# Kernel optimization log

Hardware: AMD Instinct MI355X
Metric: run time of the kernel (lower is better)

Reference implementation:

```python
import jax, jax.numpy as jnp
import numpy as np

L = 5          # num_layer
EMB = 128      # emb_dim
IN_DIM = 9     # input_dim
EDGE_DIM = 10
N_NODES = 50000
N_EDGES = 600000
N_GRAPHS = 512
BN_EPS = 1e-5


def _bn(x, g, b):
    # training-mode batch norm over axis 0 (biased variance, as torch)
    m = x.mean(axis=0)
    v = x.var(axis=0)
    return (x - m) * jax.lax.rsqrt(v + BN_EPS) * g + b


def setup_inputs() -> dict:
    key = jax.random.key(0)
    ks = jax.random.split(key, 20)
    s = 0.05
    d = {
        'x': jax.random.normal(ks[0], (N_NODES, IN_DIM), jnp.float32),
        'edge_index': jax.random.randint(ks[1], (2, N_EDGES), 0, N_NODES, jnp.int32),
        'edge_attr': jax.random.normal(ks[2], (N_EDGES, EDGE_DIM), jnp.float32),
        'batch': jnp.sort(jax.random.randint(ks[3], (N_NODES,), 0, N_GRAPHS, jnp.int32)),
        'node_W': jax.random.normal(ks[4], (IN_DIM, EMB)) * s,
        'node_b': jnp.zeros((EMB,)),
        'vn_emb': jnp.zeros((1, EMB)),                 # torch init: constant 0
        'eps': jnp.zeros((L,)),                        # GIN eps init 0
        'edge_W': jax.random.normal(ks[5], (L, EDGE_DIM, EMB)) * s,
        'edge_b': jnp.zeros((L, EMB)),
        'conv_W1': jax.random.normal(ks[6], (L, EMB, 2 * EMB)) * s,
        'conv_b1': jnp.zeros((L, 2 * EMB)),
        'conv_bn_g': jnp.ones((L, 2 * EMB)),
        'conv_bn_b': jnp.zeros((L, 2 * EMB)),
        'conv_W2': jax.random.normal(ks[7], (L, 2 * EMB, EMB)) * s,
        'conv_b2': jnp.zeros((L, EMB)),
        'bn_g': jnp.ones((L, EMB)),
        'bn_b': jnp.zeros((L, EMB)),
        'vmlp_W1': jax.random.normal(ks[8], (L - 1, EMB, 2 * EMB)) * s,
        'vmlp_b1': jnp.zeros((L - 1, 2 * EMB)),
        'vmlp_bn1_g': jnp.ones((L - 1, 2 * EMB)),
        'vmlp_bn1_b': jnp.zeros((L - 1, 2 * EMB)),
        'vmlp_W2': jax.random.normal(ks[9], (L - 1, 2 * EMB, EMB)) * s,
        'vmlp_b2': jnp.zeros((L - 1, EMB)),
        'vmlp_bn2_g': jnp.ones((L - 1, EMB)),
        'vmlp_bn2_b': jnp.zeros((L - 1, EMB)),
    }
    return d


def reference(x, edge_index, edge_attr, batch,
              node_W, node_b, vn_emb, eps, edge_W, edge_b,
              conv_W1, conv_b1, conv_bn_g, conv_bn_b, conv_W2, conv_b2,
              bn_g, bn_b,
              vmlp_W1, vmlp_b1, vmlp_bn1_g, vmlp_bn1_b,
              vmlp_W2, vmlp_b2, vmlp_bn2_g, vmlp_bn2_b):
    n = x.shape[0]
    src, dst = edge_index[0], edge_index[1]
    vn = jnp.broadcast_to(vn_emb[0], (N_GRAPHS, EMB))  # virtual node per graph
    h = x @ node_W + node_b                            # node encoder
    for l in range(L):
        h_in = h + vn[batch]                           # broadcast virtual node
        # DrugGINConv
        e = edge_attr @ edge_W[l] + edge_b[l]          # edge encoder [E,EMB]
        msg = jax.nn.relu(h_in[src] + e)               # gather + message
        agg = jax.ops.segment_sum(msg, dst, num_segments=n)  # scatter-add
        t = (1.0 + eps[l]) * h_in + agg
        t = _bn(t @ conv_W1[l] + conv_b1[l], conv_bn_g[l], conv_bn_b[l])
        t = jax.nn.relu(t) @ conv_W2[l] + conv_b2[l]
        t = _bn(t, bn_g[l], bn_b[l])                   # outer batch norm
        h = t if l == L - 1 else jax.nn.relu(t)        # dropout identity (p=0)
        if l < L - 1:
            vtmp = jax.ops.segment_sum(h_in, batch, num_segments=N_GRAPHS) + vn
            u = _bn(vtmp @ vmlp_W1[l] + vmlp_b1[l], vmlp_bn1_g[l], vmlp_bn1_b[l])
            u = jax.nn.relu(u) @ vmlp_W2[l] + vmlp_b2[l]
            vn = jax.nn.relu(_bn(u, vmlp_bn2_g[l], vmlp_bn2_b[l]))
    return h
```

## Files before the change

kernel.cpp:

```cpp
#include <hip/hip_runtime.h>


#define EMB 128
#define NGR 512
#define NLAYER 5
static constexpr float BN_EPS = 1e-5f;

typedef __attribute__((ext_vector_type(8))) short short8v;
typedef __attribute__((ext_vector_type(4))) float f32x4;

__device__ __forceinline__ ushort f2bf(float f) {
  union { float f; unsigned u; } c; c.f = f;
  return (ushort)((c.u + 0x7FFFu + ((c.u >> 16) & 1u)) >> 16);
}
__device__ __forceinline__ float bf2f(ushort h) {
  union { unsigned u; float f; } c; c.u = ((unsigned)h) << 16;
  return c.f;
}


__global__ void init_kernel(int* __restrict__ deg, int ndeg,
                            float* __restrict__ stats, int nstats,
                            float* __restrict__ vn, const float* __restrict__ vn_emb) {
  int idx = blockIdx.x * blockDim.x + threadIdx.x;
  if (idx < ndeg) deg[idx] = 0;
  if (idx < nstats) stats[idx] = 0.f;
  if (idx < NGR * EMB) vn[idx] = vn_emb[idx & (EMB - 1)];
}

__global__ void deg_kernel(const int* __restrict__ ei, int* __restrict__ deg, int E) {
  int e = blockIdx.x * blockDim.x + threadIdx.x;
  if (e < E) atomicAdd(&deg[ei[E + e]], 1);
}


__global__ void scan1_kernel(const int* __restrict__ deg, int* __restrict__ bsum, int n) {
  __shared__ int ws[4];
  int t = threadIdx.x;
  int base = blockIdx.x * 2048 + t * 8;
  int s = 0;
  #pragma unroll
  for (int i = 0; i < 8; ++i) {
    int idx = base + i;
    if (idx < n) s += deg[idx];
  }
  #pragma unroll
  for (int off = 32; off; off >>= 1) s += __shfl_down(s, off);
  if ((t & 63) == 0) ws[t >> 6] = s;
  __syncthreads();
  if (t == 0) bsum[blockIdx.x] = ws[0] + ws[1] + ws[2] + ws[3];
}

__global__ void scan2_kernel(const int* __restrict__ bsum, int* __restrict__ boff,
                             int* __restrict__ row_n, int nb) {
  int t = threadIdx.x;
  int mine = (t < nb) ? bsum[t] : 0;
  int v = mine;
  #pragma unroll
  for (int off = 1; off < 64; off <<= 1) {
    int u = __shfl_up(v, off);
    if (t >= off) v += u;
  }
  if (t < nb) boff[t] = v - mine;
  if (t == nb - 1) *row_n = v;
}

__global__ __launch_bounds__(256) void scan3_kernel(const int* __restrict__ deg,
                                                    const int* __restrict__ boff,
                                                    int* __restrict__ row_start,
                                                    int* __restrict__ cursor, int n) {
  __shared__ int lsum[256];
  int t = threadIdx.x;
  int base = blockIdx.x * 2048 + t * 8;
  int loc[8];
  int s = 0;
  #pragma unroll
  for (int i = 0; i < 8; ++i) {
    int idx = base + i;
    int d = (idx < n) ? deg[idx] : 0;
    loc[i] = s;
    s += d;
  }
  lsum[t] = s;
  __syncthreads();
  #pragma unroll
  for (int off = 1; off < 256; off <<= 1) {
    int v2 = (t >= off) ? lsum[t - off] : 0;
    __syncthreads();
    lsum[t] += v2;
    __syncthreads();
  }
  int toff = boff[blockIdx.x] + lsum[t] - s;
  #pragma unroll
  for (int i = 0; i < 8; ++i) {
    int idx = base + i;
    if (idx < n) {
      int rs = toff + loc[i];
      row_start[idx] = rs;
      cursor[idx] = rs;
    }
  }
}

__global__ void fill_kernel(const int* __restrict__ ei, int* __restrict__ cursor,
                            int2* __restrict__ el, int E) {
  int e = blockIdx.x * blockDim.x + threadIdx.x;
  if (e < E) {
    int d = ei[E + e];
    int pos = atomicAdd(&cursor[d], 1);
    el[pos] = make_int2(e, ei[e]);
  }
}

__global__ void bounds_kernel(const int* __restrict__ batch, int* __restrict__ gstart,
                              int n, int ng) {
  int g = blockIdx.x * blockDim.x + threadIdx.x;
  if (g > ng) return;
  int lo = 0, hi = n;
  while (lo < hi) {
    int mid = (lo + hi) >> 1;
    if (batch[mid] < g) lo = mid + 1; else hi = mid;
  }
  gstart[g] = lo;
}

__global__ void wtrans_kernel(const float* __restrict__ W, ushort* __restrict__ Wth,
                              ushort* __restrict__ Wtl, int K, int N, int total) {
  int idx = blockIdx.x * blockDim.x + threadIdx.x;
  if (idx >= total) return;
  int kk = idx % K;
  int t = idx / K;
  int nn = t % N;
  int l = t / N;
  float v = W[((size_t)l * K + kk) * N + nn];
  ushort h = f2bf(v);
  Wth[idx] = h;
  Wtl[idx] = f2bf(v - bf2f(h));
}

__global__ void encoder_kernel(const float* __restrict__ x, const float* __restrict__ W,
                               const float* __restrict__ b, float* __restrict__ h0, int n) {
  __shared__ float Ws[9][EMB];
  __shared__ float bs[EMB];
  int t = threadIdx.x;
  if (t < EMB) {
    #pragma unroll
    for (int k = 0; k < 9; ++k) Ws[k][t] = W[k * EMB + t];
    bs[t] = b[t];
  }
  __syncthreads();
  int total = n * EMB;
  for (int idx = blockIdx.x * blockDim.x + t; idx < total; idx += gridDim.x * blockDim.x) {
    int i = idx >> 7, j = idx & 127;
    const float* xr = x + i * 9;
    float acc = bs[j];
    #pragma unroll
    for (int k = 0; k < 9; ++k) acc = fmaf(xr[k], Ws[k][j], acc);
    h0[idx] = acc;
  }
}


template <bool RAW>
__global__ void hin_kernel(const float* __restrict__ src, const float* __restrict__ vn,
                           const int* __restrict__ batch, const float* __restrict__ s2raw,
                           const float* __restrict__ g2, const float* __restrict__ b2,
                           float* __restrict__ h_in, ushort* __restrict__ h16, int n) {
  __shared__ float sc[EMB], sh[EMB];
  if (!RAW) {
    int j = threadIdx.x;
    if (j < EMB) {
      float s = s2raw[j], q = s2raw[EMB + j];
      float mean = s / (float)n;
      float var = q / (float)n - mean * mean;
      float scl = g2[j] * rsqrtf(var + BN_EPS);
      sc[j] = scl;
      sh[j] = b2[j] - mean * scl;
    }
    __syncthreads();
  }
  int total = n * EMB;
  for (int idx = blockIdx.x * blockDim.x + threadIdx.x; idx < total; idx += gridDim.x * blockDim.x) {
    int i = idx >> 7, j = idx & 127;
    float v = src[idx];
    if (!RAW) v = fmaxf(fmaf(v, sc[j], sh[j]), 0.f);
    float hv = v + vn[batch[i] * EMB + j];
    h_in[idx] = hv;
    h16[idx] = f2bf(hv);
  }
}

__global__ void out_kernel(const float* __restrict__ t2, const float* __restrict__ s2raw,
                           const float* __restrict__ g2, const float* __restrict__ b2,
                           float* __restrict__ out, int n) {
  __shared__ float sc[EMB], sh[EMB];
  int j0 = threadIdx.x;
  if (j0 < EMB) {
    float s = s2raw[j0], q = s2raw[EMB + j0];
    float mean = s / (float)n;
    float var = q / (float)n - mean * mean;
    float scl = g2[j0] * rsqrtf(var + BN_EPS);
    sc[j0] = scl;
    sh[j0] = b2[j0] - mean * scl;
  }
  __syncthreads();
  int total = n * EMB;
  for (int idx = blockIdx.x * blockDim.x + threadIdx.x; idx < total; idx += gridDim.x * blockDim.x) {
    int j = idx & 127;
    out[idx] = fmaf(t2[idx], sc[j], sh[j]);
  }
}

__global__ void vnsum_kernel(const float* __restrict__ h_in, const int* __restrict__ gstart,
                             const float* __restrict__ vn, float* __restrict__ vnsum) {
  int g = blockIdx.x;
  int j = threadIdx.x;
  int s0 = gstart[g], s1 = gstart[g + 1];
  float acc = vn[g * EMB + j];
  for (int i = s0; i < s1; ++i) acc += h_in[i * EMB + j];
  vnsum[g * EMB + j] = acc;
}

__global__ __launch_bounds__(128) void agg_kernel(
    const float* __restrict__ h_in, const ushort* __restrict__ h16,
    const int* __restrict__ row_start, const int2* __restrict__ el,
    const float* __restrict__ edge_attr, const float* __restrict__ eW,
    const float* __restrict__ eb, const float* __restrict__ eps_p, int l,
    ushort* __restrict__ tpre_h, ushort* __restrict__ tpre_l, int n) {
  __shared__ float W[10][EMB];
  __shared__ float bia[EMB];
  int j = threadIdx.x;
  #pragma unroll
  for (int k = 0; k < 10; ++k) W[k][j] = eW[k * EMB + j];
  bia[j] = eb[j];
  float epsv = 1.f + eps_p[l];
  __syncthreads();

  int i = blockIdx.x;
  int s0 = row_start[i], s1 = row_start[i + 1];
  float acc = epsv * h_in[(size_t)i * EMB + j];
  int p = s0;
  for (; p + 4 <= s1; p += 4) {
    int2 e0 = el[p], e1 = el[p + 1], e2 = el[p + 2], e3 = el[p + 3];
    float hv0 = bf2f(h16[(size_t)e0.y * EMB + j]);
    float hv1 = bf2f(h16[(size_t)e1.y * EMB + j]);
    float hv2 = bf2f(h16[(size_t)e2.y * EMB + j]);
    float hv3 = bf2f(h16[(size_t)e3.y * EMB + j]);
    const float* ea0 = edge_attr + (size_t)e0.x * 10;
    const float* ea1 = edge_attr + (size_t)e1.x * 10;
    const float* ea2 = edge_attr + (size_t)e2.x * 10;
    const float* ea3 = edge_attr + (size_t)e3.x * 10;
    float v0 = bia[j], v1 = bia[j], v2 = bia[j], v3 = bia[j];
    #pragma unroll
    for (int k = 0; k < 10; ++k) {
      float w = W[k][j];
      v0 = fmaf(ea0[k], w, v0);
      v1 = fmaf(ea1[k], w, v1);
      v2 = fmaf(ea2[k], w, v2);
      v3 = fmaf(ea3[k], w, v3);
    }
    acc += fmaxf(v0 + hv0, 0.f) + fmaxf(v1 + hv1, 0.f) +
           fmaxf(v2 + hv2, 0.f) + fmaxf(v3 + hv3, 0.f);
  }
  for (; p < s1; ++p) {
    int2 e0 = el[p];
    float hv0 = bf2f(h16[(size_t)e0.y * EMB + j]);
    const float* ea0 = edge_attr + (size_t)e0.x * 10;
    float v0 = bia[j];
    #pragma unroll
    for (int k = 0; k < 10; ++k) v0 = fmaf(ea0[k], W[k][j], v0);
    acc += fmaxf(v0 + hv0, 0.f);
  }
  ushort hh = f2bf(acc);
  tpre_h[(size_t)i * EMB + j] = hh;
  tpre_l[(size_t)i * EMB + j] = f2bf(acc - bf2f(hh));
}

template <int KT, int NT, bool BN_A, bool STATS, bool APRE>
__global__ __launch_bounds__(256) void gemm_mfma(
    const float* __restrict__ A, const ushort* __restrict__ Ath,
    const ushort* __restrict__ Atl,
    const ushort* __restrict__ Bth, const ushort* __restrict__ Btl,
    const float* __restrict__ bias,
    float* __restrict__ C, int M,
    const float* __restrict__ bnraw, const float* __restrict__ bng,
    const float* __restrict__ bnb, float* __restrict__ statraw) {
  constexpr int BM = 128, BN = 128, BK = 32;
  constexpr int LDK = BK + 8;
  constexpr int KSTEPS = KT / BK;
  __shared__ ushort Ah[BM][LDK], Al[BM][LDK];
  __shared__ ushort Bh[BN][LDK], Bl[BN][LDK];
  __shared__ float red[8][BN], redq[8][BN];
  constexpr int SCN = BN_A ? KT : 1;
  __shared__ float scS[SCN], shS[SCN];

  int tid = threadIdx.x;
  if (BN_A) {
    for (int k = tid; k < KT; k += 256) {
      float s = bnraw[k], q = bnraw[KT + k];
      float mean = s / (float)M;
      float var = q / (float)M - mean * mean;
      float scl = bng[k] * rsqrtf(var + BN_EPS);
      scS[k] = scl;
      shS[k] = bnb[k] - mean * scl;
    }
  }

  int wv = tid >> 6, lane = tid & 63;
  int wr = wv >> 1, wc = wv & 1;
  int lr = lane & 15, kg = lane >> 4;
  int bm0 = blockIdx.x * BM;
  int gc0 = blockIdx.y * BN;

  int sr = tid >> 1;
  int skq = (tid & 1) * 16;

  f32x4 acc[4][4];
  #pragma unroll
  for (int fm = 0; fm < 4; ++fm)
    #pragma unroll
    for (int fn = 0; fn < 4; ++fn) {
      float b = bias[gc0 + wc * 64 + fn * 16 + lr];
      acc[fm][fn][0] = b; acc[fm][fn][1] = b; acc[fm][fn][2] = b; acc[fm][fn][3] = b;
    }

  for (int kt = 0; kt < KSTEPS; ++kt) {
    __syncthreads();
    {
      int grow = bm0 + sr;
      if (APRE) {
        short8v z;
        #pragma unroll
        for (int q2 = 0; q2 < 8; ++q2) z[q2] = 0;
        if (grow < M) {
          const ushort* aph = Ath + (size_t)grow * KT + kt * BK + skq;
          const ushort* apl = Atl + (size_t)grow * KT + kt * BK + skq;
          *(short8v*)&Ah[sr][skq] = *(const short8v*)aph;
          *(short8v*)&Ah[sr][skq + 8] = *(const short8v*)(aph + 8);
          *(short8v*)&Al[sr][skq] = *(const short8v*)apl;
          *(short8v*)&Al[sr][skq + 8] = *(const short8v*)(apl + 8);
        } else {
          *(short8v*)&Ah[sr][skq] = z;
          *(short8v*)&Ah[sr][skq + 8] = z;
          *(short8v*)&Al[sr][skq] = z;
          *(short8v*)&Al[sr][skq + 8] = z;
        }
      } else {
        const float* ap = A + (size_t)grow * KT + kt * BK + skq;
        short8v ah0, al0, ah1, al1;
        #pragma unroll
        for (int u = 0; u < 4; ++u) {
          float4 v = (grow < M) ? *reinterpret_cast<const float4*>(ap + u * 4)
                                : make_float4(0.f, 0.f, 0.f, 0.f);
          if (BN_A) {
            int gk = kt * BK + skq + u * 4;
            v.x = fmaxf(fmaf(v.x, scS[gk + 0], shS[gk + 0]), 0.f);
            v.y = fmaxf(fmaf(v.y, scS[gk + 1], shS[gk + 1]), 0.f);
            v.z = fmaxf(fmaf(v.z, scS[gk + 2], shS[gk + 2]), 0.f);
            v.w = fmaxf(fmaf(v.w, scS[gk + 3], shS[gk + 3]), 0.f);
          }
          float vv0 = v.x, vv1 = v.y, vv2 = v.z, vv3 = v.w;
          ushort h0 = f2bf(vv0), h1 = f2bf(vv1), h2 = f2bf(vv2), h3 = f2bf(vv3);
          ushort w0 = f2bf(vv0 - bf2f(h0)), w1 = f2bf(vv1 - bf2f(h1));
          ushort w2 = f2bf(vv2 - bf2f(h2)), w3 = f2bf(vv3 - bf2f(h3));
          if (u < 2) {
            ah0[u * 4 + 0] = (short)h0; ah0[u * 4 + 1] = (short)h1;
            ah0[u * 4 + 2] = (short)h2; ah0[u * 4 + 3] = (short)h3;
            al0[u * 4 + 0] = (short)w0; al0[u * 4 + 1] = (short)w1;
            al0[u * 4 + 2] = (short)w2; al0[u * 4 + 3] = (short)w3;
          } else {
            ah1[(u - 2) * 4 + 0] = (short)h0; ah1[(u - 2) * 4 + 1] = (short)h1;
            ah1[(u - 2) * 4 + 2] = (short)h2; ah1[(u - 2) * 4 + 3] = (short)h3;
            al1[(u - 2) * 4 + 0] = (short)w0; al1[(u - 2) * 4 + 1] = (short)w1;
            al1[(u - 2) * 4 + 2] = (short)w2; al1[(u - 2) * 4 + 3] = (short)w3;
          }
        }
        *(short8v*)&Ah[sr][skq] = ah0;
        *(short8v*)&Ah[sr][skq + 8] = ah1;
        *(short8v*)&Al[sr][skq] = al0;
        *(short8v*)&Al[sr][skq + 8] = al1;
      }
    }
    {
      const ushort* bph = Bth + (size_t)(gc0 + sr) * KT + kt * BK + skq;
      const ushort* bpl = Btl + (size_t)(gc0 + sr) * KT + kt * BK + skq;
      *(short8v*)&Bh[sr][skq] = *(const short8v*)bph;
      *(short8v*)&Bh[sr][skq + 8] = *(const short8v*)(bph + 8);
      *(short8v*)&Bl[sr][skq] = *(const short8v*)bpl;
      *(short8v*)&Bl[sr][skq + 8] = *(const short8v*)(bpl + 8);
    }
    __syncthreads();
    short8v a_h[4], a_l[4], b_h[4], b_l[4];
    #pragma unroll
    for (int f = 0; f < 4; ++f) {
      a_h[f] = *(const short8v*)&Ah[wr * 64 + f * 16 + lr][kg * 8];
      a_l[f] = *(const short8v*)&Al[wr * 64 + f * 16 + lr][kg * 8];
      b_h[f] = *(const short8v*)&Bh[wc * 64 + f * 16 + lr][kg * 8];
      b_l[f] = *(const short8v*)&Bl[wc * 64 + f * 16 + lr][kg * 8];
    }
    #pragma unroll
    for (int fm = 0; fm < 4; ++fm)
      #pragma unroll
      for (int fn = 0; fn < 4; ++fn) {
        acc[fm][fn] = __builtin_amdgcn_mfma_f32_16x16x32_bf16(a_h[fm], b_h[fn], acc[fm][fn], 0, 0, 0);
        acc[fm][fn] = __builtin_amdgcn_mfma_f32_16x16x32_bf16(a_h[fm], b_l[fn], acc[fm][fn], 0, 0, 0);
        acc[fm][fn] = __builtin_amdgcn_mfma_f32_16x16x32_bf16(a_l[fm], b_h[fn], acc[fm][fn], 0, 0, 0);
      }
  }

  #pragma unroll
  for (int fm = 0; fm < 4; ++fm) {
    int rb = bm0 + wr * 64 + fm * 16 + kg * 4;
    #pragma unroll
    for (int i = 0; i < 4; ++i) {
      int grow = rb + i;
      if (grow < M) {
        float* cp = C + (size_t)grow * NT + gc0 + wc * 64 + lr;
        #pragma unroll
        for (int fn = 0; fn < 4; ++fn) cp[fn * 16] = acc[fm][fn][i];
      }
    }
  }

  if (STATS) {
    #pragma unroll
    for (int fn = 0; fn < 4; ++fn) {
      float s = 0.f, q = 0.f;
      #pragma unroll
      for (int fm = 0; fm < 4; ++fm) {
        int rb = bm0 + wr * 64 + fm * 16 + kg * 4;
        #pragma unroll
        for (int i = 0; i < 4; ++i) {
          if (rb + i < M) {
            float v = acc[fm][fn][i];
            s += v;
            q = fmaf(v, v, q);
          }
        }
      }
      red[wr * 4 + kg][wc * 64 + fn * 16 + lr] = s;
      redq[wr * 4 + kg][wc * 64 + fn * 16 + lr] = q;
    }
    __syncthreads();
    if (tid < BN) {
      float s = 0.f, q = 0.f;
      #pragma unroll
      for (int r2 = 0; r2 < 8; ++r2) {
        s += red[r2][tid];
        q += redq[r2][tid];
      }
      int gcol = gc0 + tid;
      atomicAdd(&statraw[gcol], s);
      atomicAdd(&statraw[NT + gcol], q);
    }
  }
}


__global__ void vmlp1_kernel(const float* __restrict__ vtmp, const float* __restrict__ W,
                             const float* __restrict__ b, float* __restrict__ u1,
                             float* __restrict__ vs1raw) {
  __shared__ float a[EMB];
  int g = blockIdx.x;
  int j = threadIdx.x;
  if (j < EMB) a[j] = vtmp[g * EMB + j];
  __syncthreads();
  float acc = b[j];
  #pragma unroll 8
  for (int k = 0; k < EMB; ++k) acc = fmaf(a[k], W[k * 256 + j], acc);
  u1[g * 256 + j] = acc;
  atomicAdd(&vs1raw[j], acc);
  atomicAdd(&vs1raw[256 + j], acc * acc);
}

__global__ void vmlp2_kernel(const float* __restrict__ u1, const float* __restrict__ vs1raw,
                             const float* __restrict__ g1, const float* __restrict__ b1,
                             const float* __restrict__ W, const float* __restrict__ b2,
                             float* __restrict__ u2, float* __restrict__ vs2raw) {
  __shared__ float a[256];
  __shared__ float sc[256], sh[256];
  int g = blockIdx.x;
  int j = threadIdx.x;
  for (int k = j; k < 256; k += EMB) {
    float s = vs1raw[k], q = vs1raw[256 + k];
    float mean = s / (float)NGR;
    float var = q / (float)NGR - mean * mean;
    float scl = g1[k] * rsqrtf(var + BN_EPS);
    sc[k] = scl;
    sh[k] = b1[k] - mean * scl;
  }
  __syncthreads();
  for (int k = j; k < 256; k += EMB)
    a[k] = fmaxf(fmaf(u1[g * 256 + k], sc[k], sh[k]), 0.f);
  __syncthreads();
  float acc = b2[j];
  #pragma unroll 8
  for (int k = 0; k < 256; ++k) acc = fmaf(a[k], W[k * EMB + j], acc);
  u2[g * EMB + j] = acc;
  atomicAdd(&vs2raw[j], acc);
  atomicAdd(&vs2raw[EMB + j], acc * acc);
}

__global__ void vnupd_kernel(const float* __restrict__ u2, const float* __restrict__ vs2raw,
                             const float* __restrict__ g2, const float* __restrict__ b2,
                             float* __restrict__ vn) {
  __shared__ float sc[EMB], sh[EMB];
  int g = blockIdx.x;
  int j = threadIdx.x;
  {
    float s = vs2raw[j], q = vs2raw[EMB + j];
    float mean = s / (float)NGR;
    float var = q / (float)NGR - mean * mean;
    float scl = g2[j] * rsqrtf(var + BN_EPS);
    sc[j] = scl;
    sh[j] = b2[j] - mean * scl;
  }
  __syncthreads();
  vn[g * EMB + j] = fmaxf(fmaf(u2[g * EMB + j], sc[j], sh[j]), 0.f);
}


extern "C" void kernel_launch(void* const* d_in, const int* in_sizes, int n_in,
                              void* d_out, int out_size, void* d_ws, size_t ws_size,
                              hipStream_t stream) {
  const float* x        = (const float*)d_in[0];
  const int*   ei       = (const int*)d_in[1];
  const float* eattr    = (const float*)d_in[2];
  const int*   batch    = (const int*)d_in[3];
  const float* node_W   = (const float*)d_in[4];
  const float* node_b   = (const float*)d_in[5];
  const float* vn_emb   = (const float*)d_in[6];
  const float* eps      = (const float*)d_in[7];
  const float* edge_W   = (const float*)d_in[8];
  const float* edge_b   = (const float*)d_in[9];
  const float* conv_W1  = (const float*)d_in[10];
  const float* conv_b1  = (const float*)d_in[11];
  const float* cbn_g    = (const float*)d_in[12];
  const float* cbn_b    = (const float*)d_in[13];
  const float* conv_W2  = (const float*)d_in[14];
  const float* conv_b2  = (const float*)d_in[15];
  const float* bn_g     = (const float*)d_in[16];
  const float* bn_b     = (const float*)d_in[17];
  const float* vW1      = (const float*)d_in[18];
  const float* vb1      = (const float*)d_in[19];
  const float* vbn1_g   = (const float*)d_in[20];
  const float* vbn1_b   = (const float*)d_in[21];
  const float* vW2      = (const float*)d_in[22];
  const float* vb2      = (const float*)d_in[23];
  const float* vbn2_g   = (const float*)d_in[24];
  const float* vbn2_b   = (const float*)d_in[25];

  const int n = in_sizes[0] / 9;
  const int E = in_sizes[1] / 2;
  const int nb = (n + 2047) / 2048;

  char* p = (char*)d_ws;
  auto carve = [&](size_t bytes) {
    char* r = p;
    p += (bytes + 255) & ~(size_t)255;
    return r;
  };
  float* h_in   = (float*)carve((size_t)n * EMB * 4);
  ushort* h16   = (ushort*)carve((size_t)n * EMB * 2);
  float* t1     = (float*)carve((size_t)n * 256 * 4);
  float* t2     = (float*)carve((size_t)n * EMB * 4);
  ushort* tpre_h = (ushort*)carve((size_t)n * EMB * 2);
  ushort* tpre_l = (ushort*)carve((size_t)n * EMB * 2);
  float* vn     = (float*)carve((size_t)NGR * EMB * 4);
  float* vnsum  = (float*)carve((size_t)NGR * EMB * 4);
  float* u1     = (float*)carve((size_t)NGR * 256 * 4);
  float* u2     = (float*)carve((size_t)NGR * EMB * 4);
  float* stats  = (float*)carve((size_t)NLAYER * 1536 * 4);
  int* deg      = (int*)carve((size_t)n * 4);
  int* rstart   = (int*)carve((size_t)(n + 1) * 4);
  int* cursor   = (int*)carve((size_t)n * 4);
  int2* el      = (int2*)carve((size_t)E * 8);
  int* gstart   = (int*)carve((size_t)(NGR + 1) * 4);
  int* bsum     = (int*)carve((size_t)64 * 4);
  int* boff     = (int*)carve((size_t)64 * 4);
  ushort* wt1h  = (ushort*)carve((size_t)NLAYER * 256 * 128 * 2);
  ushort* wt1l  = (ushort*)carve((size_t)NLAYER * 256 * 128 * 2);
  ushort* wt2h  = (ushort*)carve((size_t)NLAYER * 128 * 256 * 2);
  ushort* wt2l  = (ushort*)carve((size_t)NLAYER * 128 * 256 * 2);
  float* h0     = t1;

  auto s1  = [&](int l) { return stats + (size_t)l * 1536; };
  auto s2  = [&](int l) { return stats + (size_t)l * 1536 + 512; };
  auto vs1 = [&](int l) { return stats + (size_t)l * 1536 + 768; };
  auto vs2 = [&](int l) { return stats + (size_t)l * 1536 + 1280; };

  init_kernel<<<(NGR * EMB + 255) / 256, 256, 0, stream>>>(deg, n, stats, NLAYER * 1536, vn, vn_emb);
  deg_kernel<<<(E + 255) / 256, 256, 0, stream>>>(ei, deg, E);
  scan1_kernel<<<nb, 256, 0, stream>>>(deg, bsum, n);
  scan2_kernel<<<1, 64, 0, stream>>>(bsum, boff, rstart + n, nb);
  scan3_kernel<<<nb, 256, 0, stream>>>(deg, boff, rstart, cursor, n);
  fill_kernel<<<(E + 255) / 256, 256, 0, stream>>>(ei, cursor, el, E);
  bounds_kernel<<<(NGR + 1 + 255) / 256, 256, 0, stream>>>(batch, gstart, n, NGR);
  {
    int tot1 = NLAYER * 128 * 256;
    wtrans_kernel<<<(tot1 + 255) / 256, 256, 0, stream>>>(conv_W1, wt1h, wt1l, 128, 256, tot1);
    int tot2 = NLAYER * 256 * 128;
    wtrans_kernel<<<(tot2 + 255) / 256, 256, 0, stream>>>(conv_W2, wt2h, wt2l, 256, 128, tot2);
  }
  encoder_kernel<<<2048, 256, 0, stream>>>(x, node_W, node_b, h0, n);

  const int mtiles = (n + 127) / 128;

  for (int l = 0; l < NLAYER; ++l) {
    if (l == 0)
      hin_kernel<true><<<4096, 256, 0, stream>>>(h0, vn, batch, nullptr, nullptr, nullptr,
                                                 h_in, h16, n);
    else
      hin_kernel<false><<<4096, 256, 0, stream>>>(t2, vn, batch, s2(l - 1),
                                                  bn_g + (size_t)(l - 1) * EMB,
                                                  bn_b + (size_t)(l - 1) * EMB, h_in, h16, n);
    if (l < NLAYER - 1)
      vnsum_kernel<<<NGR, EMB, 0, stream>>>(h_in, gstart, vn, vnsum);

    agg_kernel<<<n, EMB, 0, stream>>>(h_in, h16, rstart, el, eattr,
                                      edge_W + (size_t)l * 10 * EMB,
                                      edge_b + (size_t)l * EMB, eps, l, tpre_h, tpre_l, n);

    gemm_mfma<128, 256, false, true, true><<<dim3(mtiles, 2), 256, 0, stream>>>(
        nullptr, tpre_h, tpre_l, wt1h + (size_t)l * 256 * 128, wt1l + (size_t)l * 256 * 128,
        conv_b1 + (size_t)l * 256, t1, n, nullptr, nullptr, nullptr, s1(l));

    gemm_mfma<256, 128, true, true, false><<<dim3(mtiles, 1), 256, 0, stream>>>(
        t1, nullptr, nullptr, wt2h + (size_t)l * 128 * 256, wt2l + (size_t)l * 128 * 256,
        conv_b2 + (size_t)l * 128, t2, n,
        s1(l), cbn_g + (size_t)l * 256, cbn_b + (size_t)l * 256, s2(l));

    if (l < NLAYER - 1) {
      vmlp1_kernel<<<NGR, 256, 0, stream>>>(vnsum, vW1 + (size_t)l * 128 * 256,
                                            vb1 + (size_t)l * 256, u1, vs1(l));
      vmlp2_kernel<<<NGR, EMB, 0, stream>>>(u1, vs1(l), vbn1_g + (size_t)l * 256,
                                            vbn1_b + (size_t)l * 256,
                                            vW2 + (size_t)l * 256 * 128,
                                            vb2 + (size_t)l * EMB, u2, vs2(l));
      vnupd_kernel<<<NGR, EMB, 0, stream>>>(u2, vs2(l), vbn2_g + (size_t)l * EMB,
                                            vbn2_b + (size_t)l * EMB, vn);
    }
  }

  out_kernel<<<4096, 256, 0, stream>>>(t2, s2(NLAYER - 1),
                                       bn_g + (size_t)(NLAYER - 1) * EMB,
                                       bn_b + (size_t)(NLAYER - 1) * EMB,
                                       (float*)d_out, n);
}
```

Before: 1.280 ms.

## Pack edge source and bf16 edge attributes into CSR-ordered records

The CSR fill step now writes a 32-byte record per edge holding the source index and the ten edge attributes rounded to bf16, stored in destination order. The aggregation kernel reads these contiguous records instead of chasing edge ids into the fp32 edge_attr array. The main loop is also unrolled to 8 edges so more neighbour-row gathers are in flight at once. This cuts scattered memory traffic across five layers, at the cost of bf16 precision on edge attributes and extra register pressure.

After: 1.271 ms. Within noise of the previous version (-0.8%).

```diff
diff --git a/kernel.cpp b/kernel.cpp
--- a/kernel.cpp
+++ b/kernel.cpp
@@ -17,6 +17,12 @@
   union { unsigned u; float f; } c; c.u = ((unsigned)h) << 16;
   return c.f;
 }
+
+struct __attribute__((aligned(32))) EPack {
+  int src;
+  ushort ea[10];
+  ushort pad[3];
+};
 
 
 __global__ void init_kernel(int* __restrict__ deg, int ndeg,
@@ -103,12 +109,19 @@
 }
 
 __global__ void fill_kernel(const int* __restrict__ ei, int* __restrict__ cursor,
-                            int2* __restrict__ el, int E) {
+                            const float* __restrict__ eattr,
+                            EPack* __restrict__ epk, int E) {
   int e = blockIdx.x * blockDim.x + threadIdx.x;
   if (e < E) {
     int d = ei[E + e];
     int pos = atomicAdd(&cursor[d], 1);
-    el[pos] = make_int2(e, ei[e]);
+    EPack r;
+    r.src = ei[e];
+    const float* ea = eattr + (size_t)e * 10;
+    #pragma unroll
+    for (int k = 0; k < 10; ++k) r.ea[k] = f2bf(ea[k]);
+    r.pad[0] = r.pad[1] = r.pad[2] = 0;
+    epk[pos] = r;
   }
 }
 
@@ -223,9 +236,9 @@
 
 __global__ __launch_bounds__(128) void agg_kernel(
     const float* __restrict__ h_in, const ushort* __restrict__ h16,
-    const int* __restrict__ row_start, const int2* __restrict__ el,
-    const float* __restrict__ edge_attr, const float* __restrict__ eW,
-    const float* __restrict__ eb, const float* __restrict__ eps_p, int l,
+    const int* __restrict__ row_start, const EPack* __restrict__ epk,
+    const float* __restrict__ eW, const float* __restrict__ eb,
+    const float* __restrict__ eps_p, int l,
     ushort* __restrict__ tpre_h, ushort* __restrict__ tpre_l, int n) {
   __shared__ float W[10][EMB];
   __shared__ float bia[EMB];
@@ -240,36 +253,45 @@
   int s0 = row_start[i], s1 = row_start[i + 1];
   float acc = epsv * h_in[(size_t)i * EMB + j];
   int p = s0;
+  for (; p + 8 <= s1; p += 8) {
+    int srcs[8];
+    #pragma unroll
+    for (int u = 0; u < 8; ++u) srcs[u] = epk[p + u].src;
+    float hv[8];
+    #pragma unroll
+    for (int u = 0; u < 8; ++u) hv[u] = bf2f(h16[(size_t)srcs[u] * EMB + j]);
+    #pragma unroll
+    for (int u = 0; u < 8; ++u) {
+      const EPack* ep = epk + p + u;
+      float v = bia[j];
+      #pragma unroll
+      for (int k = 0; k < 10; ++k) v = fmaf(bf2f(ep->ea[k]), W[k][j], v);
+      acc += fmaxf(v + hv[u], 0.f);
+    }
+  }
   for (; p + 4 <= s1; p += 4) {
-    int2 e0 = el[p], e1 = el[p + 1], e2 = el[p + 2], e3 = el[p + 3];
-    float hv0 = bf2f(h16[(size_t)e0.y * EMB + j]);
-    float hv1 = bf2f(h16[(size_t)e1.y * EMB + j]);
-    float hv2 = bf2f(h16[(size_t)e2.y * EMB + j]);
-    float hv3 = bf2f(h16[(size_t)e3.y * EMB + j]);
-    const float* ea0 = edge_attr + (size_t)e0.x * 10;
-    const float* ea1 = edge_attr + (size_t)e1.x * 10;
-    const float* ea2 = edge_attr + (size_t)e2.x * 10;
-    const float* ea3 = edge_attr + (size_t)e3.x * 10;
-    float v0 = bia[j], v1 = bia[j], v2 = bia[j], v3 = bia[j];
-    #pragma unroll
-    for (int k = 0; k < 10; ++k) {
-      float w = W[k][j];
-      v0 = fmaf(ea0[k], w, v0);
-      v1 = fmaf(ea1[k], w, v1);
-      v2 = fmaf(ea2[k], w, v2);
-      v3 = fmaf(ea3[k], w, v3);
-    }
-    acc += fmaxf(v0 + hv0, 0.f) + fmaxf(v1 + hv1, 0.f) +
-           fmaxf(v2 + hv2, 0.f) + fmaxf(v3 + hv3, 0.f);
+    int srcs[4];
+    #pragma unroll
+    for (int u = 0; u < 4; ++u) srcs[u] = epk[p + u].src;
+    float hv[4];
+    #pragma unroll
+    for (int u = 0; u < 4; ++u) hv[u] = bf2f(h16[(size_t)srcs[u] * EMB + j]);
+    #pragma unroll
+    for (int u = 0; u < 4; ++u) {
+      const EPack* ep = epk + p + u;
+      float v = bia[j];
+      #pragma unroll
+      for (int k = 0; k < 10; ++k) v = fmaf(bf2f(ep->ea[k]), W[k][j], v);
+      acc += fmaxf(v + hv[u], 0.f);
+    }
   }
   for (; p < s1; ++p) {
-    int2 e0 = el[p];
-    float hv0 = bf2f(h16[(size_t)e0.y * EMB + j]);
-    const float* ea0 = edge_attr + (size_t)e0.x * 10;
-    float v0 = bia[j];
-    #pragma unroll
-    for (int k = 0; k < 10; ++k) v0 = fmaf(ea0[k], W[k][j], v0);
-    acc += fmaxf(v0 + hv0, 0.f);
+    const EPack* ep = epk + p;
+    float hv0 = bf2f(h16[(size_t)ep->src * EMB + j]);
+    float v = bia[j];
+    #pragma unroll
+    for (int k = 0; k < 10; ++k) v = fmaf(bf2f(ep->ea[k]), W[k][j], v);
+    acc += fmaxf(v + hv0, 0.f);
   }
   ushort hh = f2bf(acc);
   tpre_h[(size_t)i * EMB + j] = hh;
@@ -574,7 +596,7 @@
   int* deg      = (int*)carve((size_t)n * 4);
   int* rstart   = (int*)carve((size_t)(n + 1) * 4);
   int* cursor   = (int*)carve((size_t)n * 4);
-  int2* el      = (int2*)carve((size_t)E * 8);
+  EPack* epk    = (EPack*)carve((size_t)E * sizeof(EPack));
   int* gstart   = (int*)carve((size_t)(NGR + 1) * 4);
   int* bsum     = (int*)carve((size_t)64 * 4);
   int* boff     = (int*)carve((size_t)64 * 4);
@@ -594,7 +616,7 @@
   scan1_kernel<<<nb, 256, 0, stream>>>(deg, bsum, n);
   scan2_kernel<<<1, 64, 0, stream>>>(bsum, boff, rstart + n, nb);
   scan3_kernel<<<nb, 256, 0, stream>>>(deg, boff, rstart, cursor, n);
-  fill_kernel<<<(E + 255) / 256, 256, 0, stream>>>(ei, cursor, el, E);
+  fill_kernel<<<(E + 255) / 256, 256, 0, stream>>>(ei, cursor, eattr, epk, E);
   bounds_kernel<<<(NGR + 1 + 255) / 256, 256, 0, stream>>>(batch, gstart, n, NGR);
   {
     int tot1 = NLAYER * 128 * 256;
@@ -617,7 +639,7 @@
     if (l < NLAYER - 1)
       vnsum_kernel<<<NGR, EMB, 0, stream>>>(h_in, gstart, vn, vnsum);
 
-    agg_kernel<<<n, EMB, 0, stream>>>(h_in, h16, rstart, el, eattr,
+    agg_kernel<<<n, EMB, 0, stream>>>(h_in, h16, rstart, epk,
                                       edge_W + (size_t)l * 10 * EMB,
                                       edge_b + (size_t)l * EMB, eps, l, tpre_h, tpre_l, n);
 
```
